# Kernel optimization log

Measured on AMD Instinct MI355X. Metric: run time of the kernel, lower is better.

## Reference

```python
import jax, jax.numpy as jnp
import numpy as np

V = 30000      # vocab_size
D = 300        # t_embed
H = 4          # GATv2 heads
C = 300        # per-head out channels (hidden_dim = t_embed)
HID = 768      # hidden_size
B = 2
T = 800
NEG = 0.2      # GATv2 negative_slope default


def gatv2_layer(x, src, dst, Wl, bl, Wr, br, att, bias):
    """PyG GATv2Conv, eval mode, add_self_loops=True, concat=True.
    x: [N, Fin]; src/dst: [E] (src->dst message flow).
    Wl/Wr: [Fin, H*C]; bl/br: [H*C]; att: [H, C]; bias: [H*C].
    """
    N = x.shape[0]
    xl = (x @ Wl + bl).reshape(N, H, C)   # source transform
    xr = (x @ Wr + br).reshape(N, H, C)   # target transform
    loops = jnp.arange(N)
    s = jnp.concatenate([src, loops])
    d = jnp.concatenate([dst, loops])
    e = jax.nn.leaky_relu(xl[s] + xr[d], NEG)          # [E', H, C]
    logits = jnp.einsum('ehc,hc->eh', e, att)           # [E', H]
    # scatter-softmax over incoming edges per target node
    mx = jax.ops.segment_max(logits, d, num_segments=N)  # [N, H]
    ex = jnp.exp(logits - mx[d])
    den = jax.ops.segment_sum(ex, d, num_segments=N)
    alpha = ex / den[d]                                   # [E', H]
    out = jax.ops.segment_sum(alpha[:, :, None] * xl[s], d, num_segments=N)
    return out.reshape(N, H * C) + bias


def setup_inputs() -> dict:
    key = jax.random.key(0)
    ks = jax.random.split(key, 20)
    sc = 0.05
    inp = {
        'kg_enc_input': jax.random.randint(ks[0], (B, T, 3), 0, V),
        'embeddings': jax.random.normal(ks[1], (V, D), jnp.float32),
        # conv1: GATv2Conv(D, C, heads=H)
        'Wl1': jax.random.normal(ks[2], (D, H * C), jnp.float32) * sc,
        'bl1': jnp.zeros((H * C,), jnp.float32),
        'Wr1': jax.random.normal(ks[3], (D, H * C), jnp.float32) * sc,
        'br1': jnp.zeros((H * C,), jnp.float32),
        'att1': jax.random.normal(ks[4], (H, C), jnp.float32) * sc,
        'bias1': jnp.zeros((H * C,), jnp.float32),
        # conv2: GATv2Conv(4*C, C, heads=H)
        'Wl2': jax.random.normal(ks[5], (H * C, H * C), jnp.float32) * sc,
        'bl2': jnp.zeros((H * C,), jnp.float32),
        'Wr2': jax.random.normal(ks[6], (H * C, H * C), jnp.float32) * sc,
        'br2': jnp.zeros((H * C,), jnp.float32),
        'att2': jax.random.normal(ks[7], (H, C), jnp.float32) * sc,
        'bias2': jnp.zeros((H * C,), jnp.float32),
        # post_mp: Linear(4*C, C) -> Dropout -> Linear(C, D)
        'Wp1': jax.random.normal(ks[8], (H * C, C), jnp.float32) * sc,
        'bp1': jnp.zeros((C,), jnp.float32),
        'Wp2': jax.random.normal(ks[9], (C, D), jnp.float32) * sc,
        'bp2': jnp.zeros((D,), jnp.float32),
        # lii: Linear(3*D, HID, bias=False)
        'Wlii': jax.random.normal(ks[10], (3 * D, HID), jnp.float32) * sc,
    }
    return inp


def reference(kg_enc_input, embeddings, Wl1, bl1, Wr1, br1, att1, bias1,
              Wl2, bl2, Wr2, br2, att2, bias2, Wp1, bp1, Wp2, bp2, Wlii):
    # original GAT.forward detaches x -> no grad to embedding table
    x0 = jax.lax.stop_gradient(embeddings)

    def per_sample(kg):  # kg: [T, 3]
        head, rel, tail = kg[:, 0], kg[:, 1], kg[:, 2]
        # edge_list = cat([[head;rel], [rel;tail]], dim=1)
        src = jnp.concatenate([head, rel])
        dst = jnp.concatenate([rel, tail])
        h = gatv2_layer(x0, src, dst, Wl1, bl1, Wr1, br1, att1, bias1)
        h = jax.nn.relu(h)                 # dropout: eval mode, identity
        h = gatv2_layer(h, src, dst, Wl2, bl2, Wr2, br2, att2, bias2)
        h = jax.nn.relu(h)
        w = (h @ Wp1 + bp1) @ Wp2 + bp2    # post_mp, [V, D]
        # per-triple gather + concat of (h, r, t) node embeddings
        return jnp.concatenate([w[head], w[rel], w[tail]], axis=-1)  # [T, 3D]

    final = jax.vmap(per_sample)(kg_enc_input)   # [B, T, 3D]
    return final @ Wlii                           # [B, T, HID]
```

## Files before the change

### kernel.cpp

```cpp
#include <hip/hip_runtime.h>
#include <hip/hip_bf16.h>

#define V 30000
#define D 300
#define H 4
#define C 300
#define HC 1200
#define B 2
#define T 800
#define E 1600
#define MAXM 2400
#define NEG 0.2f
#define SCAN_CH ((MAXM + 255) / 256)

#define MR 2432
#define KD 320
#define KHC 1216
#define NLR 2432
#define WB_LD 320
#define KF2 960

typedef __attribute__((ext_vector_type(8))) unsigned short u16x8;
typedef __attribute__((ext_vector_type(8))) short s16x8;
typedef __attribute__((ext_vector_type(4))) float f32x4;

__device__ inline unsigned short f2b(float v) {
    unsigned u = __float_as_uint(v);
    unsigned r = (u + 0x7FFFu + ((u >> 16) & 1u)) >> 16;
    return (unsigned short)r;
}
__device__ inline float b2f(unsigned short u) {
    return __uint_as_float(((unsigned)u) << 16);
}

#define GLOAD_LDS16(g, l) __builtin_amdgcn_global_load_lds( \
    (const __attribute__((address_space(1))) void*)(g), \
    (__attribute__((address_space(3))) void*)(l), 16, 0, 0)


__global__ void k_mark(const int* __restrict__ kg, int* map) {
    int i = blockIdx.x * blockDim.x + threadIdx.x;
    if (i >= B * T * 3) return;
    int b = i / (T * 3);
    map[b * V + kg[i]] = 1;
}

__global__ void k_compact(int* map, int* list, int* mcnt) {
    int b = blockIdx.y;
    int i = blockIdx.x * 256 + threadIdx.x;
    bool pred = (i < V) && (map[b * V + i] == 1);
    unsigned long long m = __ballot(pred);
    int lane = threadIdx.x & 63;
    int wid = threadIdx.x >> 6;
    __shared__ int wcnt[4];
    __shared__ int base;
    if (lane == 0) wcnt[wid] = __popcll(m);
    __syncthreads();
    if (threadIdx.x == 0) {
        int t = 0;
#pragma unroll
        for (int w2 = 0; w2 < 4; ++w2) { int c = wcnt[w2]; wcnt[w2] = t; t += c; }
        base = t ? atomicAdd(&mcnt[b], t) : 0;
    }
    __syncthreads();
    if (pred) {
        int idx = base + wcnt[wid] + __popcll(m & ((1ull << lane) - 1ull));
        map[b * V + i] = idx;
        list[b * MAXM + idx] = i;
    }
}

__global__ __launch_bounds__(256) void k_graph(const int* __restrict__ kg,
                                               const int* __restrict__ map,
                                               int* __restrict__ off_g,
                                               int* __restrict__ csr,
                                               int* __restrict__ tric) {
    int b = blockIdx.x;
    int tid = threadIdx.x;
    __shared__ int sdeg[MAXM];
    __shared__ int soff[MAXM + 1];
    __shared__ int ses[E];
    __shared__ int sed[E];
    __shared__ int ts[256];
    for (int j = tid; j < MAXM; j += 256) sdeg[j] = 0;
    __syncthreads();
    for (int t = tid; t < T; t += 256) {
        const int* kk = kg + ((long)b * T + t) * 3;
        int hc = map[b * V + kk[0]];
        int rc = map[b * V + kk[1]];
        int tc = map[b * V + kk[2]];
        ses[t] = hc;     sed[t] = rc;
        ses[T + t] = rc; sed[T + t] = tc;
        atomicAdd(&sdeg[rc], 1);
        atomicAdd(&sdeg[tc], 1);
        int* tr = tric + ((long)b * T + t) * 3;
        tr[0] = hc; tr[1] = rc; tr[2] = tc;
    }
    __syncthreads();
    int base = tid * SCAN_CH;
    int loc[SCAN_CH];
    int sum = 0;
#pragma unroll
    for (int j = 0; j < SCAN_CH; ++j) {
        int v = (base + j < MAXM) ? sdeg[base + j] : 0;
        sum += v; loc[j] = sum;
    }
    ts[tid] = sum; __syncthreads();
    for (int s = 1; s < 256; s <<= 1) {
        int v = (tid >= s) ? ts[tid - s] : 0;
        __syncthreads();
        ts[tid] += v;
        __syncthreads();
    }
    int excl = (tid > 0) ? ts[tid - 1] : 0;
#pragma unroll
    for (int j = 0; j < SCAN_CH; ++j)
        if (base + j < MAXM) soff[base + j + 1] = excl + loc[j];
    if (tid == 0) soff[0] = 0;
    __syncthreads();
    for (int j = tid; j < MAXM; j += 256) sdeg[j] = 0;
    __syncthreads();
    for (int e = tid; e < E; e += 256) {
        int d = sed[e];
        int pos = soff[d] + atomicAdd(&sdeg[d], 1);
        csr[b * E + pos] = ses[e];
    }
    for (int j = tid; j <= MAXM; j += 256) off_g[b * (MAXM + 1) + j] = soff[j];
}

__global__ void k_wt_all(const float* __restrict__ Wl1, const float* __restrict__ Wr1,
                         const float* __restrict__ Wl2, const float* __restrict__ Wr2,
                         const float* __restrict__ Wp1, const float* __restrict__ Wp2,
                         const float* __restrict__ Wlii,
                         const float* __restrict__ bl1, const float* __restrict__ br1,
                         const float* __restrict__ bl2, const float* __restrict__ br2,
                         const float* __restrict__ bp1, const float* __restrict__ bp2,
                         unsigned short* Wlr1t, unsigned short* Wlr2t,
                         unsigned short* Wp2t, unsigned short* Wp1b,
                         unsigned short* Wft2,
                         float* blr1, float* blr2, float* bp12) {
    const int KT[6]  = {10, 10, 38, 38, 10, 30};
    const int CUM[10] = {0, 380, 760, 2204, 3648, 3748, 4468, 4508, 4518, 4520};
    int bid = blockIdx.x;
    int task = 0;
    while (bid >= CUM[task + 1]) ++task;
    int local = bid - CUM[task];
    int tx = threadIdx.x, ty = threadIdx.y;
    int tid = ty * 32 + tx;

    if (task == 6) {
        int r0 = local * 32;
#pragma unroll
        for (int p = 0; p < 4; ++p) {
            int row = r0 + ty + p * 8;
#pragma unroll
            for (int j = 0; j < 10; ++j) {
                int c = tx + j * 32;
                unsigned short v = 0;
                if (row < 1200 && c < 300) v = f2b(Wp1[(long)row * 300 + c]);
                Wp1b[(long)row * 320 + c] = v;
            }
        }
        return;
    }
    if (task == 7) {
        int c = local * 256 + tid;
        if (c < NLR) {
            float v1 = 0.f, v2 = 0.f;
            if (c < 1200) { v1 = bl1[c]; v2 = bl2[c]; }
            else if (c >= 1216 && c < 2416) { v1 = br1[c - 1216]; v2 = br2[c - 1216]; }
            blr1[c] = v1; blr2[c] = v2;
        }
        return;
    }
    if (task == 8) {
        int n = local * 256 + tid;
        if (n < 300) {
            float s = bp2[n];
            for (int m = 0; m < 300; ++m) s += bp1[m] * Wp2[(long)m * 300 + n];
            bp12[n] = s;
        }
        return;
    }

    __shared__ float t[32][33];
    if (task == 5) {
        int kt = local % 30, nt = local / 30;
        int k0 = kt * 32, n0 = nt * 32;
#pragma unroll
        for (int p = 0; p < 4; ++p) {
            int gk = k0 + ty + p * 8, n = n0 + tx;
            int pp = (gk >= 640) ? 2 : (gk >= 320 ? 1 : 0);
            int kc = gk - pp * 320;
            t[ty + p * 8][tx] = (kc < 300) ? Wlii[(long)(300 * pp + kc) * 768 + n] : 0.f;
        }
        __syncthreads();
#pragma unroll
        for (int p = 0; p < 4; ++p) {
            int n = n0 + ty + p * 8, gk = k0 + tx;
            Wft2[(long)n * 960 + gk] = f2b(t[tx][ty + p * 8]);
        }
        return;
    }

    int kt = local % KT[task], nt = local / KT[task];
    const float* W; unsigned short* Wt; int K, N, Kp;
    switch (task) {
        case 0: W = Wl1;  Wt = Wlr1t;                     K = 300;  N = 1200; Kp = KD;  break;
        case 1: W = Wr1;  Wt = Wlr1t + (long)1216 * KD;   K = 300;  N = 1200; Kp = KD;  break;
        case 2: W = Wl2;  Wt = Wlr2t;                     K = 1200; N = 1200; Kp = KHC; break;
        case 3: W = Wr2;  Wt = Wlr2t + (long)1216 * KHC;  K = 1200; N = 1200; Kp = KHC; break;
        default: W = Wp2; Wt = Wp2t;                      K = 300;  N = 300;  Kp = KD;  break;
    }
    int k0 = kt * 32, n0 = nt * 32;
#pragma unroll
    for (int p = 0; p < 4; ++p) {
        int k = k0 + ty + p * 8, n = n0 + tx;
        t[ty + p * 8][tx] = (k < K && n < N) ? W[(long)k * N + n] : 0.f;
    }
    __syncthreads();
#pragma unroll
    for (int p = 0; p < 4; ++p) {
        int n = n0 + ty + p * 8, k = k0 + tx;
        Wt[(long)n * Kp + k] = f2b(t[tx][ty + p * 8]);
    }
}

__global__ void k_embgather(const float* __restrict__ emb, const int* __restrict__ list,
                            unsigned short* __restrict__ Eb) {
    int b = blockIdx.y, i = blockIdx.x;
    int src = list[b * MAXM + i];
    const float* e = emb + (long)src * D;
    unsigned short* o = Eb + ((long)b * MR + i) * KD;
    int c = threadIdx.x;
    if (c < 75) {
        float4 v = *(const float4*)(e + c * 4);
        ushort4 u;
        u.x = f2b(v.x); u.y = f2b(v.y); u.z = f2b(v.z); u.w = f2b(v.w);
        *(ushort4*)(o + c * 4) = u;
    } else if (c < 80) {
        *(ushort4*)(o + c * 4) = make_ushort4(0, 0, 0, 0);
    }
}

__device__ inline void tile_decode(int& m0, int& n0) {
    int nbx = gridDim.x, nby = gridDim.y;
    int nwg = nbx * nby;
    int wg = blockIdx.y * nbx + blockIdx.x;
    int q = nwg >> 3, r8 = nwg & 7;
    int xcd = wg & 7, idx = wg >> 3;
    int L = (xcd < r8 ? xcd * (q + 1) : r8 * (q + 1) + (xcd - r8) * q) + idx;
    const int G = 4;
    int band = L / (G * nbx);
    int first = band * G;
    int sz = min(G, nby - first);
    int rem = L - band * G * nbx;
    int by = first + rem % sz;
    int bx = rem / sz;
    m0 = by * 128; n0 = bx * 128;
}

__global__ __launch_bounds__(256) void k_mgemm(
    const unsigned short* __restrict__ A, long sA, int lda,
    const unsigned short* __restrict__ Wt, int ldw,
    const float* __restrict__ bias,
    int N, int K,
    unsigned short* __restrict__ outB, long sB, int ldb_) {
    int b = blockIdx.z;
    A += (long)b * sA;
    __shared__ unsigned short lds[3 * 8192];
    int tid = threadIdx.x;
    int m0, n0; tile_decode(m0, n0);

    int w = tid >> 6, lane = tid & 63;
    int wr = (w >> 1) * 64, wc = (w & 1) * 64;
    int fr = lane & 15, fq = lane >> 4;
    int r0 = tid >> 2, sg = tid & 3;
    int swz = (sg ^ ((r0 >> 1) & 3)) * 8;
    const unsigned short* Ap  = A  + (long)(m0 + r0) * lda + swz;
    const unsigned short* Ap2 = A  + (long)(m0 + r0 + 64) * lda + swz;
    const unsigned short* Bp  = Wt + (long)(n0 + r0) * ldw + swz;
    const unsigned short* Bp2 = Wt + (long)(n0 + r0 + 64) * ldw + swz;

    auto stage = [&](int buf, int k0) {
        unsigned short* a_ = lds + buf * 4096;
        unsigned short* b_ = lds + 12288 + buf * 4096;
        GLOAD_LDS16(Ap + k0,  a_ + r0 * 32 + sg * 8);
        GLOAD_LDS16(Ap2 + k0, a_ + (r0 + 64) * 32 + sg * 8);
        GLOAD_LDS16(Bp + k0,  b_ + r0 * 32 + sg * 8);
        GLOAD_LDS16(Bp2 + k0, b_ + (r0 + 64) * 32 + sg * 8);
    };

    f32x4 acc[4][4] = {};
    int NT = K >> 5;
    stage(0, 0);
    stage(1, 32);
    int cur = 0, stg = 2;
    for (int i = 0; i < NT; ++i) {
        if (i + 1 < NT) asm volatile("s_waitcnt vmcnt(4)" ::: "memory");
        else            asm volatile("s_waitcnt vmcnt(0)" ::: "memory");
        __builtin_amdgcn_s_barrier();
        __builtin_amdgcn_sched_barrier(0);
        if (i + 2 < NT) stage(stg, (i + 2) << 5);
        const unsigned short* a_ = lds + cur * 4096;
        const unsigned short* b_ = lds + 12288 + cur * 4096;
        s16x8 af[4], bfr[4];
#pragma unroll
        for (int m = 0; m < 4; ++m) {
            int rr = wr + m * 16 + fr;
            af[m] = *(const s16x8*)&a_[rr * 32 + (fq ^ ((rr >> 1) & 3)) * 8];
        }
#pragma unroll
        for (int n = 0; n < 4; ++n) {
            int rr = wc + n * 16 + fr;
            bfr[n] = *(const s16x8*)&b_[rr * 32 + (fq ^ ((rr >> 1) & 3)) * 8];
        }
#pragma unroll
        for (int m = 0; m < 4; ++m)
#pragma unroll
            for (int n = 0; n < 4; ++n)
                acc[m][n] = __builtin_amdgcn_mfma_f32_16x16x32_bf16(af[m], bfr[n], acc[m][n], 0, 0, 0);
        cur = (cur == 2) ? 0 : cur + 1;
        stg = (stg == 2) ? 0 : stg + 1;
    }
    __syncthreads();
#pragma unroll
    for (int m = 0; m < 4; ++m) {
        int rl = wr + m * 16 + fq * 4;
#pragma unroll
        for (int n = 0; n < 4; ++n) {
            int cl = wc + n * 16 + fr;
            int colg = n0 + cl;
            float bi = (colg < N && bias) ? bias[colg] : 0.f;
#pragma unroll
            for (int j = 0; j < 4; ++j) {
                unsigned short v = (colg < N) ? f2b(acc[m][n][j] + bi) : (unsigned short)0;
                lds[(rl + j) * 128 + cl] = v;
            }
        }
    }
    __syncthreads();
    unsigned short* oB = outB + (long)b * sB;
#pragma unroll
    for (int q = 0; q < 8; ++q) {
        int idx = q * 256 + tid;
        int row = idx >> 4, c8 = idx & 15;
        int colg = n0 + c8 * 8;
        if (colg < ldb_)
            *(u16x8*)(oB + (long)(m0 + row) * ldb_ + colg) = *(const u16x8*)&lds[row * 128 + c8 * 8];
    }
}

__global__ __launch_bounds__(256) void k_fgemm(
    const unsigned short* __restrict__ wb, long sW,
    const int* __restrict__ tric,
    const unsigned short* __restrict__ Wft2,
    float* __restrict__ out) {
    int b = blockIdx.z;
    const unsigned short* wB = wb + (long)b * sW;
    const int* tr = tric + (long)b * T * 3;
    float* oF = out + (long)b * T * 768;
    __shared__ unsigned short lds[3 * 8192];
    int tid = threadIdx.x;
    int m0, n0; tile_decode(m0, n0);

    int w = tid >> 6, lane = tid & 63;
    int wr = (w >> 1) * 64, wc = (w & 1) * 64;
    int fr = lane & 15, fq = lane >> 4;
    int r0 = tid >> 2, sg = tid & 3;
    int swz = (sg ^ ((r0 >> 1) & 3)) * 8;

    int gm  = m0 + r0;
    int gm2 = gm + 64;
    int t1 = min(gm, T - 1) * 3, t2 = min(gm2, T - 1) * 3;
    int tr_a[3] = {tr[t1], tr[t1 + 1], tr[t1 + 2]};
    int tr_b[3] = {tr[t2], tr[t2 + 1], tr[t2 + 2]};

    const unsigned short* Bp  = Wft2 + (long)(n0 + r0) * KF2 + swz;
    const unsigned short* Bp2 = Wft2 + (long)(n0 + r0 + 64) * KF2 + swz;

    auto stage = [&](int buf, int k0) {
        unsigned short* a_ = lds + buf * 4096;
        unsigned short* b_ = lds + 12288 + buf * 4096;
        int kk = k0 + swz;
        int p_ = (kk >= 640) ? 2 : (kk >= 320 ? 1 : 0);
        int kc = kk - p_ * 320;
        GLOAD_LDS16(wB + (long)tr_a[p_] * WB_LD + kc, a_ + r0 * 32 + sg * 8);
        GLOAD_LDS16(wB + (long)tr_b[p_] * WB_LD + kc, a_ + (r0 + 64) * 32 + sg * 8);
        GLOAD_LDS16(Bp + k0,  b_ + r0 * 32 + sg * 8);
        GLOAD_LDS16(Bp2 + k0, b_ + (r0 + 64) * 32 + sg * 8);
    };

    f32x4 acc[4][4] = {};
    const int NT = KF2 >> 5;
    stage(0, 0);
    stage(1, 32);
    int cur = 0, stg = 2;
    for (int i = 0; i < NT; ++i) {
        if (i + 1 < NT) asm volatile("s_waitcnt vmcnt(4)" ::: "memory");
        else            asm volatile("s_waitcnt vmcnt(0)" ::: "memory");
        __builtin_amdgcn_s_barrier();
        __builtin_amdgcn_sched_barrier(0);
        if (i + 2 < NT) stage(stg, (i + 2) << 5);
        const unsigned short* a_ = lds + cur * 4096;
        const unsigned short* b_ = lds + 12288 + cur * 4096;
        s16x8 af[4], bfr[4];
#pragma unroll
        for (int m = 0; m < 4; ++m) {
            int rr = wr + m * 16 + fr;
            af[m] = *(const s16x8*)&a_[rr * 32 + (fq ^ ((rr >> 1) & 3)) * 8];
        }
#pragma unroll
        for (int n = 0; n < 4; ++n) {
            int rr = wc + n * 16 + fr;
            bfr[n] = *(const s16x8*)&b_[rr * 32 + (fq ^ ((rr >> 1) & 3)) * 8];
        }
#pragma unroll
        for (int m = 0; m < 4; ++m)
#pragma unroll
            for (int n = 0; n < 4; ++n)
                acc[m][n] = __builtin_amdgcn_mfma_f32_16x16x32_bf16(af[m], bfr[n], acc[m][n], 0, 0, 0);
        cur = (cur == 2) ? 0 : cur + 1;
        stg = (stg == 2) ? 0 : stg + 1;
    }
#pragma unroll
    for (int m = 0; m < 4; ++m) {
        int rb = m0 + wr + m * 16 + fq * 4;
#pragma unroll
        for (int n = 0; n < 4; ++n) {
            int col = n0 + wc + n * 16 + fr;
#pragma unroll
            for (int j = 0; j < 4; ++j) {
                int row = rb + j;
                if (row < T) oF[(long)row * 768 + col] = acc[m][n][j];
            }
        }
    }
}

__global__ __launch_bounds__(256) void k_att(
    const unsigned short* __restrict__ XLR,
    const int* __restrict__ off, const int* __restrict__ csr,
    const float* __restrict__ att, const float* __restrict__ bias,
    unsigned short* __restrict__ OUT) {
    const long sX = (long)MR * NLR;
    const long sO = (long)MR * KHC;
    int b = blockIdx.y;
    int i = blockIdx.x;
    const unsigned short* xl = XLR + (long)b * sX;
    const unsigned short* xr = xl + 1216;
    unsigned short* out = OUT + (long)b * sO;
    int lane = threadIdx.x & 63;
    int h = threadIdx.x >> 6;
    int c0 = lane * 4;
    int c1 = 256 + c0;
    bool tail = lane < 11;

    float xrf[8], attf[8];
    {
        const unsigned short* xp = xr + (long)i * NLR + h * C;
        ushort4 u0 = *(const ushort4*)(xp + c0);
        ushort4 u1 = tail ? *(const ushort4*)(xp + c1) : make_ushort4(0, 0, 0, 0);
        xrf[0] = b2f(u0.x); xrf[1] = b2f(u0.y); xrf[2] = b2f(u0.z); xrf[3] = b2f(u0.w);
        xrf[4] = b2f(u1.x); xrf[5] = b2f(u1.y); xrf[6] = b2f(u1.z); xrf[7] = b2f(u1.w);
        float4 a0 = *(const float4*)(att + h * C + c0);
        attf[0] = a0.x; attf[1] = a0.y; attf[2] = a0.z; attf[3] = a0.w;
        if (tail) {
            float4 a1 = *(const float4*)(att + h * C + c1);
            attf[4] = a1.x; attf[5] = a1.y; attf[6] = a1.z; attf[7] = a1.w;
        } else { attf[4] = attf[5] = attf[6] = attf[7] = 0.f; }
    }
    int o0 = off[b * (MAXM + 1) + i];
    int dg = off[b * (MAXM + 1) + i + 1] - o0;
    const int* cs = csr + b * E;

    float mx = -3e38f, den = 0.f;
    float acc[8] = {0.f, 0.f, 0.f, 0.f, 0.f, 0.f, 0.f, 0.f};
    auto step = [&](int s) {
        const unsigned short* xp = xl + (long)s * NLR + h * C;
        ushort4 v0 = *(const ushort4*)(xp + c0);
        ushort4 v1 = tail ? *(const ushort4*)(xp + c1) : make_ushort4(0, 0, 0, 0);
        float xv[8];
        xv[0] = b2f(v0.x); xv[1] = b2f(v0.y); xv[2] = b2f(v0.z); xv[3] = b2f(v0.w);
        xv[4] = b2f(v1.x); xv[5] = b2f(v1.y); xv[6] = b2f(v1.z); xv[7] = b2f(v1.w);
        float part = 0.f;
#pragma unroll
        for (int j = 0; j < 8; ++j) {
            float v = xv[j] + xrf[j];
            v = v > 0.f ? v : NEG * v;
            part += attf[j] * v;
        }
#pragma unroll
        for (int m = 1; m < 64; m <<= 1) part += __shfl_xor(part, m);
        float mn = fmaxf(mx, part);
        float sc = __expf(mx - mn);
        float p = __expf(part - mn);
        den = den * sc + p;
#pragma unroll
        for (int j = 0; j < 8; ++j) acc[j] = acc[j] * sc + p * xv[j];
        mx = mn;
    };
    step(i);
    for (int e = 0; e < dg; ++e) step(cs[o0 + e]);

    float inv = 1.f / den;
    unsigned short* op = out + (long)i * KHC + h * C;
    {
        float4 b0 = *(const float4*)(bias + h * C + c0);
        ushort4 s0;
        float v;
        v = acc[0] * inv + b0.x; s0.x = f2b(v > 0.f ? v : 0.f);
        v = acc[1] * inv + b0.y; s0.y = f2b(v > 0.f ? v : 0.f);
        v = acc[2] * inv + b0.z; s0.z = f2b(v > 0.f ? v : 0.f);
        v = acc[3] * inv + b0.w; s0.w = f2b(v > 0.f ? v : 0.f);
        *(ushort4*)(op + c0) = s0;
        if (tail) {
            float4 b1 = *(const float4*)(bias + h * C + c1);
            ushort4 s1;
            v = acc[4] * inv + b1.x; s1.x = f2b(v > 0.f ? v : 0.f);
            v = acc[5] * inv + b1.y; s1.y = f2b(v > 0.f ? v : 0.f);
            v = acc[6] * inv + b1.z; s1.z = f2b(v > 0.f ? v : 0.f);
            v = acc[7] * inv + b1.w; s1.w = f2b(v > 0.f ? v : 0.f);
            *(ushort4*)(op + c1) = s1;
        }
    }
    if (h == 0 && lane < KHC - HC)
        out[(long)i * KHC + HC + lane] = 0;
}

extern "C" void kernel_launch(void* const* d_in, const int* in_sizes, int n_in,
                              void* d_out, int out_size, void* d_ws, size_t ws_size,
                              hipStream_t stream) {
    const int*   kg    = (const int*)d_in[0];
    const float* emb   = (const float*)d_in[1];
    const float* Wl1   = (const float*)d_in[2];
    const float* bl1   = (const float*)d_in[3];
    const float* Wr1   = (const float*)d_in[4];
    const float* br1   = (const float*)d_in[5];
    const float* att1  = (const float*)d_in[6];
    const float* bias1 = (const float*)d_in[7];
    const float* Wl2   = (const float*)d_in[8];
    const float* bl2   = (const float*)d_in[9];
    const float* Wr2   = (const float*)d_in[10];
    const float* br2   = (const float*)d_in[11];
    const float* att2  = (const float*)d_in[12];
    const float* bias2 = (const float*)d_in[13];
    const float* Wp1   = (const float*)d_in[14];
    const float* bp1   = (const float*)d_in[15];
    const float* Wp2   = (const float*)d_in[16];
    const float* bp2   = (const float*)d_in[17];
    const float* Wlii  = (const float*)d_in[18];
    float* out = (float*)d_out;

    char* ws = (char*)d_ws;
    size_t o = 0;
    auto alloc = [&](size_t bytes) -> void* {
        void* p = ws + o;
        o = (o + bytes + 255) & ~(size_t)255;
        return p;
    };
    int* map  = (int*)alloc(sizeof(int) * B * V);
    int* list = (int*)alloc(sizeof(int) * B * MAXM);
    int* mcnt = (int*)alloc(sizeof(int) * B);
    int* off  = (int*)alloc(sizeof(int) * B * (MAXM + 1));
    int* csr  = (int*)alloc(sizeof(int) * B * E);
    int* tric = (int*)alloc(sizeof(int) * B * T * 3);

    long sXlr = (long)MR * NLR;
    long sHb  = (long)MR * KHC;
    long sEb  = (long)MR * KD;
    unsigned short* Xlr = (unsigned short*)alloc(2LL * B * sXlr);
    unsigned short* Hb  = (unsigned short*)alloc(2LL * B * sHb);
    unsigned short* Eb  = (unsigned short*)alloc(2LL * B * sEb);

    unsigned short* Wlr1t = (unsigned short*)alloc(2LL * 2432 * KD);
    unsigned short* Wlr2t = (unsigned short*)alloc(2LL * 2432 * KHC);
    unsigned short* Wp2t  = (unsigned short*)alloc(2LL * 384 * KD);
    unsigned short* Wp1b  = (unsigned short*)alloc(2LL * 1280 * 320);
    unsigned short* Wp12t = (unsigned short*)alloc(2LL * 384 * KHC);
    unsigned short* Wft2  = (unsigned short*)alloc(2LL * 768 * KF2);
    float* blr1 = (float*)alloc(sizeof(float) * NLR);
    float* blr2 = (float*)alloc(sizeof(float) * NLR);
    float* bp12 = (float*)alloc(sizeof(float) * 384);
    (void)ws_size; (void)in_sizes; (void)n_in; (void)out_size;

    unsigned short* wb = Eb;

    hipMemsetAsync(map, 0xFF, sizeof(int) * B * V, stream);
    hipMemsetAsync(list, 0, sizeof(int) * B * MAXM, stream);
    hipMemsetAsync(mcnt, 0, sizeof(int) * B, stream);
    k_mark<<<(B * T * 3 + 255) / 256, 256, 0, stream>>>(kg, map);
    k_compact<<<dim3((V + 255) / 256, B), 256, 0, stream>>>(map, list, mcnt);
    k_graph<<<B, 256, 0, stream>>>(kg, map, off, csr, tric);

    k_wt_all<<<4520, dim3(32, 8), 0, stream>>>(Wl1, Wr1, Wl2, Wr2, Wp1, Wp2, Wlii,
                                               bl1, br1, bl2, br2, bp1, bp2,
                                               Wlr1t, Wlr2t, Wp2t, Wp1b, Wft2,
                                               blr1, blr2, bp12);

    k_embgather<<<dim3(MAXM, B), 128, 0, stream>>>(emb, list, Eb);

    k_mgemm<<<dim3(10, 3, 1), 256, 0, stream>>>(Wp2t, 0, KD, Wp1b, 320, nullptr,
                                                1216, KD, Wp12t, 0, KHC);

    long sWb = (long)MR * WB_LD;

    dim3 gL(19, 19, B);
    k_mgemm<<<gL, 256, 0, stream>>>(Eb, sEb, KD, Wlr1t, KD, blr1,
                                    NLR, KD, Xlr, sXlr, NLR);
    k_att<<<dim3(MAXM, B), 256, 0, stream>>>(Xlr, off, csr, att1, bias1, Hb);
    k_mgemm<<<gL, 256, 0, stream>>>(Hb, sHb, KHC, Wlr2t, KHC, blr2,
                                    NLR, KHC, Xlr, sXlr, NLR);
    k_att<<<dim3(MAXM, B), 256, 0, stream>>>(Xlr, off, csr, att2, bias2, Hb);
    k_mgemm<<<dim3(3, 19, B), 256, 0, stream>>>(Hb, sHb, KHC, Wp12t, KHC, bp12,
                                                300, KHC, wb, sWb, WB_LD);
    k_fgemm<<<dim3(6, 7, B), 256, 0, stream>>>(wb, sWb, tric, Wft2, out);
}
```

Before: 284.0 us.

## Enlarge GEMM tile to 256x128 with padded epilogue staging

The generic bf16 MFMA GEMM now computes 256x128 output tiles, with each wave owning a 128x64 sub-tile and holding 8x4 accumulators. This halves the grid in M and doubles A reuse per B fragment. Row padding (MR) grows to 2560 so full tiles stay in bounds, and a new Mstore bound clips the stores. The epilogue LDS stride is padded to 136 to reduce bank conflicts. Costs are more registers and LDS per block, fewer blocks (lower occupancy and weaker tail balance), and extra wasted rows on the padded tiles.

```diff
diff --git a/kernel.cpp b/kernel.cpp
--- a/kernel.cpp
+++ b/kernel.cpp
@@ -13,7 +13,7 @@
 #define NEG 0.2f
 #define SCAN_CH ((MAXM + 255) / 256)
 
-#define MR 2432
+#define MR 2560
 #define KD 320
 #define KHC 1216
 #define NLR 2432
@@ -243,7 +243,17 @@
     }
 }
 
-__device__ inline void tile_decode(int& m0, int& n0) {
+__global__ __launch_bounds__(256) void k_mgemm(
+    const unsigned short* __restrict__ A, long sA, int lda,
+    const unsigned short* __restrict__ Wt, int ldw,
+    const float* __restrict__ bias,
+    int N, int K, int Mstore,
+    unsigned short* __restrict__ outB, long sB, int ldb_) {
+    int b = blockIdx.z;
+    A += (long)b * sA;
+    __shared__ unsigned short lds[36864];
+    int tid = threadIdx.x;
+
     int nbx = gridDim.x, nby = gridDim.y;
     int nwg = nbx * nby;
     int wg = blockIdx.y * nbx + blockIdx.x;
@@ -257,97 +267,100 @@
     int rem = L - band * G * nbx;
     int by = first + rem % sz;
     int bx = rem / sz;
-    m0 = by * 128; n0 = bx * 128;
-}
-
-__global__ __launch_bounds__(256) void k_mgemm(
-    const unsigned short* __restrict__ A, long sA, int lda,
-    const unsigned short* __restrict__ Wt, int ldw,
-    const float* __restrict__ bias,
-    int N, int K,
-    unsigned short* __restrict__ outB, long sB, int ldb_) {
-    int b = blockIdx.z;
-    A += (long)b * sA;
-    __shared__ unsigned short lds[3 * 8192];
-    int tid = threadIdx.x;
-    int m0, n0; tile_decode(m0, n0);
+    int m0 = by * 256, n0 = bx * 128;
 
     int w = tid >> 6, lane = tid & 63;
-    int wr = (w >> 1) * 64, wc = (w & 1) * 64;
+    int wm = (w >> 1) * 128, wn = (w & 1) * 64;
     int fr = lane & 15, fq = lane >> 4;
     int r0 = tid >> 2, sg = tid & 3;
-    int swz = (sg ^ ((r0 >> 1) & 3)) * 8;
-    const unsigned short* Ap  = A  + (long)(m0 + r0) * lda + swz;
-    const unsigned short* Ap2 = A  + (long)(m0 + r0 + 64) * lda + swz;
-    const unsigned short* Bp  = Wt + (long)(n0 + r0) * ldw + swz;
-    const unsigned short* Bp2 = Wt + (long)(n0 + r0 + 64) * ldw + swz;
+
+    const unsigned short* ApR0; const unsigned short* ApR1;
+    const unsigned short* ApR2; const unsigned short* ApR3;
+    {
+        int row = r0;
+        ApR0 = A + (long)(m0 + row) * lda + (sg ^ ((row >> 1) & 3)) * 8;
+        row = r0 + 64;
+        ApR1 = A + (long)(m0 + row) * lda + (sg ^ ((row >> 1) & 3)) * 8;
+        row = r0 + 128;
+        ApR2 = A + (long)(m0 + row) * lda + (sg ^ ((row >> 1) & 3)) * 8;
+        row = r0 + 192;
+        ApR3 = A + (long)(m0 + row) * lda + (sg ^ ((row >> 1) & 3)) * 8;
+    }
+    const unsigned short* BpR0; const unsigned short* BpR1;
+    {
+        int row = r0;
+        BpR0 = Wt + (long)(n0 + row) * ldw + (sg ^ ((row >> 1) & 3)) * 8;
+        row = r0 + 64;
+        BpR1 = Wt + (long)(n0 + row) * ldw + (sg ^ ((row >> 1) & 3)) * 8;
+    }
 
     auto stage = [&](int buf, int k0) {
-        unsigned short* a_ = lds + buf * 4096;
-        unsigned short* b_ = lds + 12288 + buf * 4096;
-        GLOAD_LDS16(Ap + k0,  a_ + r0 * 32 + sg * 8);
-        GLOAD_LDS16(Ap2 + k0, a_ + (r0 + 64) * 32 + sg * 8);
-        GLOAD_LDS16(Bp + k0,  b_ + r0 * 32 + sg * 8);
-        GLOAD_LDS16(Bp2 + k0, b_ + (r0 + 64) * 32 + sg * 8);
+        unsigned short* a_ = lds + buf * 8192;
+        unsigned short* b_ = lds + 24576 + buf * 4096;
+        GLOAD_LDS16(ApR0 + k0, a_ + r0 * 32 + sg * 8);
+        GLOAD_LDS16(ApR1 + k0, a_ + (r0 + 64) * 32 + sg * 8);
+        GLOAD_LDS16(ApR2 + k0, a_ + (r0 + 128) * 32 + sg * 8);
+        GLOAD_LDS16(ApR3 + k0, a_ + (r0 + 192) * 32 + sg * 8);
+        GLOAD_LDS16(BpR0 + k0, b_ + r0 * 32 + sg * 8);
+        GLOAD_LDS16(BpR1 + k0, b_ + (r0 + 64) * 32 + sg * 8);
     };
 
-    f32x4 acc[4][4] = {};
+    f32x4 acc[8][4] = {};
     int NT = K >> 5;
     stage(0, 0);
     stage(1, 32);
     int cur = 0, stg = 2;
     for (int i = 0; i < NT; ++i) {
-        if (i + 1 < NT) asm volatile("s_waitcnt vmcnt(4)" ::: "memory");
+        if (i + 1 < NT) asm volatile("s_waitcnt vmcnt(6)" ::: "memory");
         else            asm volatile("s_waitcnt vmcnt(0)" ::: "memory");
         __builtin_amdgcn_s_barrier();
         __builtin_amdgcn_sched_barrier(0);
         if (i + 2 < NT) stage(stg, (i + 2) << 5);
-        const unsigned short* a_ = lds + cur * 4096;
-        const unsigned short* b_ = lds + 12288 + cur * 4096;
-        s16x8 af[4], bfr[4];
-#pragma unroll
-        for (int m = 0; m < 4; ++m) {
-            int rr = wr + m * 16 + fr;
-            af[m] = *(const s16x8*)&a_[rr * 32 + (fq ^ ((rr >> 1) & 3)) * 8];
-        }
+        const unsigned short* a_ = lds + cur * 8192;
+        const unsigned short* b_ = lds + 24576 + cur * 4096;
+        s16x8 bfr[4];
 #pragma unroll
         for (int n = 0; n < 4; ++n) {
-            int rr = wc + n * 16 + fr;
+            int rr = wn + n * 16 + fr;
             bfr[n] = *(const s16x8*)&b_[rr * 32 + (fq ^ ((rr >> 1) & 3)) * 8];
         }
 #pragma unroll
-        for (int m = 0; m < 4; ++m)
+        for (int m = 0; m < 8; ++m) {
+            int rr = wm + m * 16 + fr;
+            s16x8 af = *(const s16x8*)&a_[rr * 32 + (fq ^ ((rr >> 1) & 3)) * 8];
 #pragma unroll
             for (int n = 0; n < 4; ++n)
-                acc[m][n] = __builtin_amdgcn_mfma_f32_16x16x32_bf16(af[m], bfr[n], acc[m][n], 0, 0, 0);
+                acc[m][n] = __builtin_amdgcn_mfma_f32_16x16x32_bf16(af, bfr[n], acc[m][n], 0, 0, 0);
+        }
         cur = (cur == 2) ? 0 : cur + 1;
         stg = (stg == 2) ? 0 : stg + 1;
     }
     __syncthreads();
 #pragma unroll
-    for (int m = 0; m < 4; ++m) {
-        int rl = wr + m * 16 + fq * 4;
+    for (int m = 0; m < 8; ++m) {
+        int rl = wm + m * 16 + fq * 4;
 #pragma unroll
         for (int n = 0; n < 4; ++n) {
-            int cl = wc + n * 16 + fr;
+            int cl = wn + n * 16 + fr;
             int colg = n0 + cl;
             float bi = (colg < N && bias) ? bias[colg] : 0.f;
 #pragma unroll
             for (int j = 0; j < 4; ++j) {
                 unsigned short v = (colg < N) ? f2b(acc[m][n][j] + bi) : (unsigned short)0;
-                lds[(rl + j) * 128 + cl] = v;
+                lds[(rl + j) * 136 + cl] = v;
             }
         }
     }
     __syncthreads();
     unsigned short* oB = outB + (long)b * sB;
 #pragma unroll
-    for (int q = 0; q < 8; ++q) {
-        int idx = q * 256 + tid;
-        int row = idx >> 4, c8 = idx & 15;
+    for (int qq = 0; qq < 16; ++qq) {
+        int idx2 = qq * 256 + tid;
+        int row = idx2 >> 4, c8 = idx2 & 15;
         int colg = n0 + c8 * 8;
-        if (colg < ldb_)
-            *(u16x8*)(oB + (long)(m0 + row) * ldb_ + colg) = *(const u16x8*)&lds[row * 128 + c8 * 8];
+        int rowg = m0 + row;
+        if (colg < ldb_ && rowg < Mstore)
+            *(u16x8*)(oB + (long)rowg * ldb_ + colg) = *(const u16x8*)&lds[row * 136 + c8 * 8];
     }
 }
 
@@ -362,7 +375,20 @@
     float* oF = out + (long)b * T * 768;
     __shared__ unsigned short lds[3 * 8192];
     int tid = threadIdx.x;
-    int m0, n0; tile_decode(m0, n0);
+    int nbx = gridDim.x, nby = gridDim.y;
+    int nwg = nbx * nby;
+    int wg = blockIdx.y * nbx + blockIdx.x;
+    int q = nwg >> 3, r8 = nwg & 7;
+    int xcd = wg & 7, idx = wg >> 3;
+    int L = (xcd < r8 ? xcd * (q + 1) : r8 * (q + 1) + (xcd - r8) * q) + idx;
+    const int G = 4;
+    int band = L / (G * nbx);
+    int first = band * G;
+    int sz = min(G, nby - first);
+    int rem = L - band * G * nbx;
+    int by = first + rem % sz;
+    int bx = rem / sz;
+    int m0 = by * 128, n0 = bx * 128;
 
     int w = tid >> 6, lane = tid & 63;
     int wr = (w >> 1) * 64, wc = (w & 1) * 64;
@@ -600,19 +626,19 @@
 
     k_embgather<<<dim3(MAXM, B), 128, 0, stream>>>(emb, list, Eb);
 
-    k_mgemm<<<dim3(10, 3, 1), 256, 0, stream>>>(Wp2t, 0, KD, Wp1b, 320, nullptr,
-                                                1216, KD, Wp12t, 0, KHC);
+    k_mgemm<<<dim3(10, 2, 1), 256, 0, stream>>>(Wp2t, 0, KD, Wp1b, 320, nullptr,
+                                                1216, KD, 384, Wp12t, 0, KHC);
 
     long sWb = (long)MR * WB_LD;
 
-    dim3 gL(19, 19, B);
+    dim3 gL(19, 10, B);
     k_mgemm<<<gL, 256, 0, stream>>>(Eb, sEb, KD, Wlr1t, KD, blr1,
-                                    NLR, KD, Xlr, sXlr, NLR);
+                                    NLR, KD, MR, Xlr, sXlr, NLR);
     k_att<<<dim3(MAXM, B), 256, 0, stream>>>(Xlr, off, csr, att1, bias1, Hb);
     k_mgemm<<<gL, 256, 0, stream>>>(Hb, sHb, KHC, Wlr2t, KHC, blr2,
-                                    NLR, KHC, Xlr, sXlr, NLR);
+                                    NLR, KHC, MR, Xlr, sXlr, NLR);
     k_att<<<dim3(MAXM, B), 256, 0, stream>>>(Xlr, off, csr, att2, bias2, Hb);
-    k_mgemm<<<dim3(3, 19, B), 256, 0, stream>>>(Hb, sHb, KHC, Wp12t, KHC, bp12,
-                                                300, KHC, wb, sWb, WB_LD);
+    k_mgemm<<<dim3(3, 10, B), 256, 0, stream>>>(Hb, sHb, KHC, Wp12t, KHC, bp12,
+                                                300, KHC, MR, wb, sWb, WB_LD);
     k_fgemm<<<dim3(6, 7, B), 256, 0, stream>>>(wb, sWb, tric, Wft2, out);
 }
```

Result: slower. 327.8 us (+15.4%).
